# Kernel optimization log

Measured on AMD Instinct MI355X. Metric: run time of the kernel, lower is better.

The kernel has to match this reference:

```python
import jax, jax.numpy as jnp
import numpy as np

TAU = 2.0   # LIF membrane time constant
VTH = 1.0   # spike threshold
EPS = 1e-5
T = 2       # spiking timesteps
H = 8       # attention heads
L = 4       # transformer depth
SCALE = 0.125
GW = 0.8    # graph branch weight


def _spike(v):
    # heaviside forward, sigmoid surrogate backward (spikingjelly-style)
    sg = jax.nn.sigmoid(4.0 * (v - VTH))
    return sg + jax.lax.stop_gradient((v >= VTH).astype(v.dtype) - sg)


def lif(x):
    # multi-step LIF over leading time axis, hard reset, detach_reset=True
    def step(v, xt):
        v = v + (xt - v) / TAU
        s = _spike(v)
        v = v * (1.0 - jax.lax.stop_gradient(s))
        return v, s
    _, s = jax.lax.scan(step, jnp.zeros_like(x[0]), x)
    return s


def bn(x, g, b):
    # batch-norm (training stats) over all dims but the channel dim
    ax = tuple(range(x.ndim - 1))
    m = x.mean(ax, keepdims=True)
    v = x.var(ax, keepdims=True)
    return (x - m) * jax.lax.rsqrt(v + EPS) * g + b


def ln(x, g, b):
    m = x.mean(-1, keepdims=True)
    v = x.var(-1, keepdims=True)
    return (x - m) * jax.lax.rsqrt(v + EPS) * g + b


def gcn_agg(x, row, col, n):
    # symmetric-normalized sparse aggregation: out[col] += x[row] / sqrt(d[row]d[col])
    deg = jax.ops.segment_sum(jnp.ones_like(col, dtype=x.dtype), col, num_segments=n)
    dinv = jnp.where(deg > 0, jax.lax.rsqrt(deg), 0.0)
    val = dinv[col] * dinv[row]
    return jax.ops.segment_sum(val[:, None] * x[row], col, num_segments=n)


def _forward(fl, edge_index):
    (x, fc0_w, fc0_b, ln_g, ln_b, wq, wk, wv, wo,
     bnq_g, bnq_b, bnk_g, bnk_b, bnv_g, bnv_b, bno_g, bno_b,
     w1, bn1_g, bn1_b, w2, bn2_g, bn2_b, head_w, head_b,
     gfc_w, gfc_b, gbn0_g, gbn0_b, gconv_w, gconv_b, gbn_g, gbn_b,
     fc_w, fc_b) = fl
    N = x.shape[0]
    row, col = edge_index[0], edge_index[1]
    # ---- spiking transformer branch: x -> [T,N,D] ----
    h = jnp.broadcast_to(x, (T,) + x.shape) @ fc0_w + fc0_b
    h = jax.nn.relu(ln(h, ln_g, ln_b))
    D = h.shape[-1]
    for l in range(L):
        s = lif(h)
        q = lif(bn(s @ wq[l], bnq_g[l], bnq_b[l])).reshape(T, N, H, D // H)
        k = lif(bn(s @ wk[l], bnk_g[l], bnk_b[l])).reshape(T, N, H, D // H)
        v = lif(bn(s @ wv[l], bnv_g[l], bnv_b[l])).reshape(T, N, H, D // H)
        # linear (token-sum) spiking self-attention: kv = K^T V per head/timestep
        kv = jnp.einsum('tnhd,tnhe->thde', k, v)
        o = (jnp.einsum('tnhd,thde->tnhe', q, kv) * SCALE).reshape(T, N, D)
        o = bn(lif(o) @ wo[l], bno_g[l], bno_b[l])
        h = h + o
        m = bn(lif(h) @ w1[l], bn1_g[l], bn1_b[l])
        m = bn(lif(m) @ w2[l], bn2_g[l], bn2_b[l])
        h = h + m
    x1 = (lif(h) @ head_w + head_b).mean(0)   # [N, C], mean over T (TET=False)
    # ---- sparse GNN diffusion branch ----
    g0 = jax.nn.relu(bn(x @ gfc_w + gfc_b, gbn0_g, gbn0_b))
    g = g0
    for i in range(2):
        g = gcn_agg(g, row, col, N) @ gconv_w[i] + gconv_b[i]
        g = jax.nn.relu(bn(g, gbn_g[i], gbn_b[i]))
        g = g + g0  # residual to first layer
    out = GW * g + (1.0 - GW) * x1
    return out @ fc_w + fc_b


def setup_inputs() -> dict:
    key = jax.random.key(0)
    ks = iter(jax.random.split(key, 64))
    N, F, D, C = 16384, 512, 512, 40
    DH = 2 * D
    r = lambda *s: jax.random.normal(next(ks), s, dtype=jnp.float32)
    inp = {
        'x': r(N, F),
        'fc0_w': r(F, D) * 0.02, 'fc0_b': jnp.zeros((D,), jnp.float32),
        'ln_g': jnp.ones((D,), jnp.float32), 'ln_b': jnp.zeros((D,), jnp.float32),
        'wq': r(L, D, D) * 0.02, 'wk': r(L, D, D) * 0.02,
        'wv': r(L, D, D) * 0.02, 'wo': r(L, D, D) * 0.02,
        'bnq_g': 1.0 + 0.1 * r(L, D), 'bnq_b': 0.02 * r(L, D),
        'bnk_g': 1.0 + 0.1 * r(L, D), 'bnk_b': 0.02 * r(L, D),
        'bnv_g': 1.0 + 0.1 * r(L, D), 'bnv_b': 0.02 * r(L, D),
        'bno_g': 1.0 + 0.1 * r(L, D), 'bno_b': 0.02 * r(L, D),
        'w1': r(L, D, DH) * 0.02, 'bn1_g': 1.0 + 0.1 * r(L, DH), 'bn1_b': 0.02 * r(L, DH),
        'w2': r(L, DH, D) * 0.02, 'bn2_g': 1.0 + 0.1 * r(L, D), 'bn2_b': 0.02 * r(L, D),
        'head_w': r(D, C) * 0.02, 'head_b': jnp.zeros((C,), jnp.float32),
        'gfc_w': r(F, C) * 0.02, 'gfc_b': jnp.zeros((C,), jnp.float32),
        'gbn0_g': jnp.ones((C,), jnp.float32), 'gbn0_b': jnp.zeros((C,), jnp.float32),
        'gconv_w': r(2, C, C) * 0.1, 'gconv_b': jnp.zeros((2, C), jnp.float32),
        'gbn_g': 1.0 + 0.1 * r(2, C), 'gbn_b': 0.02 * r(2, C),
        'fc_w': r(C, C) * 0.1, 'fc_b': jnp.zeros((C,), jnp.float32),
        'edge_index': jax.random.randint(next(ks), (2, 262144), 0, N, dtype=jnp.int32),
    }
    return inp


def reference(x, fc0_w, fc0_b, ln_g, ln_b, wq, wk, wv, wo, bnq_g, bnq_b, bnk_g, bnk_b, bnv_g, bnv_b, bno_g, bno_b, w1, bn1_g, bn1_b, w2, bn2_g, bn2_b, head_w, head_b, gfc_w, gfc_b, gbn0_g, gbn0_b, gconv_w, gconv_b, gbn_g, gbn_b, fc_w, fc_b, edge_index):
    fl = (x, fc0_w, fc0_b, ln_g, ln_b, wq, wk, wv, wo, bnq_g, bnq_b, bnk_g, bnk_b, bnv_g, bnv_b, bno_g, bno_b, w1, bn1_g, bn1_b, w2, bn2_g, bn2_b, head_w, head_b, gfc_w, gfc_b, gbn0_g, gbn0_b, gconv_w, gconv_b, gbn_g, gbn_b, fc_w, fc_b)
    return _forward(fl, edge_index)
```

## Files before the change

### kernel.cpp

```cpp
#include <hip/hip_runtime.h>
#include <cstddef>
#include <cstdint>

constexpr int N_NODES = 16384;
constexpr int D_MODEL = 512;
constexpr int C_OUT   = 40;
constexpr int CW      = 256;
constexpr int ND      = N_NODES * D_MODEL;
constexpr int M2      = 2 * N_NODES;

typedef int i32x4 __attribute__((ext_vector_type(4)));

#define S0 0.001953125
#define S1 1.52587890625e-05
#define S2 1.1920928955078125e-07
#define S3 9.31322574615478515625e-10
#define S4 7.2759576141834259033203125e-12

#define WD_Q 0
#define WD_K 1310720
#define WD_V 2621440
#define WD_O 3932160
#define WD_1 5242880
#define WD_2 7864320
#define WD_TOTAL 10485760

__global__ __launch_bounds__(256)
void w_digits_layer(const float* __restrict__ wq, const float* __restrict__ wk,
                    const float* __restrict__ wv, const float* __restrict__ wo,
                    const float* __restrict__ w1, const float* __restrict__ w2,
                    uint8_t* __restrict__ Wd) {
    int idx = blockIdx.x * 256 + threadIdx.x;
    const float* W;
    uint8_t* outb;
    int N, rem;
    if (idx < 65536) {
        int mm = idx >> 14;
        rem = idx & 16383;
        const float* ptrs[4] = {wq, wk, wv, wo};
        W = ptrs[mm]; outb = Wd + (size_t)mm * 1310720; N = 512;
    } else if (idx < 98304) {
        rem = idx - 65536; W = w1; outb = Wd + WD_1; N = 1024;
    } else {
        rem = idx - 98304; W = w2; outb = Wd + WD_2; N = 512;
    }
    int kg = rem / N, n = rem - kg * N;
    const float* Wp = W + (size_t)kg * 16 * N + n;
    uint8_t* out = outb + (size_t)(kg * N + n) * 80;
    const double scl[5] = {512.0, 65536.0, 8388608.0, 1073741824.0, 137438953472.0};
    const double inv[5] = {S0, S1, S2, S3, S4};
    union { uint8_t b[5][16]; i32x4 v[5]; } db;
#pragma unroll
    for (int kk = 0; kk < 16; ++kk) {
        double r = (double)Wp[(size_t)kk * N];
#pragma unroll
        for (int j = 0; j < 5; ++j) {
            int d = (int)rint(r * scl[j]);
            d = d > 127 ? 127 : (d < -127 ? -127 : d);
            r -= (double)d * inv[j];
            db.b[j][kk] = (uint8_t)(int8_t)d;
        }
    }
#pragma unroll
    for (int j = 0; j < 5; ++j)
        *reinterpret_cast<i32x4*>(out + j * 16) = db.v[j];
}

__global__ __launch_bounds__(256)
void gemm_i8_bits(const uint64_t* __restrict__ bits, int kWords,
                  const uint8_t* __restrict__ Wd, int Nmat, int colOff,
                  float* __restrict__ C, int ldc, int K,
                  double* __restrict__ sum, double* __restrict__ sumsq) {
    __shared__ __attribute__((aligned(16))) uint8_t Bs[20480];
    const int lane = threadIdx.x & 63;
    const int wv   = threadIdx.x >> 6;
    const int m    = lane & 15;
    const int q    = lane >> 4;
    const int rowT = blockIdx.y * 128 + wv * 32;
    const int colB = blockIdx.x * 64;

    i32x4 acc[2][4][5];
#pragma unroll
    for (int rt = 0; rt < 2; ++rt)
#pragma unroll
        for (int t = 0; t < 4; ++t)
#pragma unroll
            for (int j = 0; j < 5; ++j) acc[rt][t][j] = (i32x4){0, 0, 0, 0};

    const uint64_t* brow0 = bits + (size_t)(rowT + m) * kWords;
    const uint64_t* brow1 = brow0 + (size_t)16 * kWords;
    const size_t cb = (size_t)(colOff + colB);

    for (int kb = 0; kb < K; kb += 64) {
        i32x4 tmp[5];
        const size_t kt0 = (size_t)(kb >> 4);
#pragma unroll
        for (int c5 = 0; c5 < 5; ++c5) {
            int c  = threadIdx.x + c5 * 256;
            int kt = c / 320;
            int of = c - kt * 320;
            tmp[c5] = *reinterpret_cast<const i32x4*>(
                Wd + ((kt0 + (size_t)kt) * Nmat + cb) * 80 + (size_t)of * 16);
        }
        uint64_t wb0 = brow0[kb >> 6];
        uint64_t wb1 = brow1[kb >> 6];
        uint32_t hw0 = (uint32_t)(wb0 >> (q * 16)) & 0xFFFFu;
        uint32_t hw1 = (uint32_t)(wb1 >> (q * 16)) & 0xFFFFu;
        i32x4 af0, af1;
#pragma unroll
        for (int i = 0; i < 4; ++i) {
            af0[i] = (int)((((hw0 >> (4 * i)) & 0xFu) * 0x00204081u) & 0x01010101u);
            af1[i] = (int)((((hw1 >> (4 * i)) & 0xFu) * 0x00204081u) & 0x01010101u);
        }
        __syncthreads();
#pragma unroll
        for (int c5 = 0; c5 < 5; ++c5) {
            int c  = threadIdx.x + c5 * 256;
            int kt = c / 320;
            int of = c - kt * 320;
            *reinterpret_cast<i32x4*>(Bs + kt * 5120 + of * 16) = tmp[c5];
        }
        __syncthreads();
#pragma unroll
        for (int t = 0; t < 4; ++t) {
            const uint8_t* bt = Bs + q * 5120 + (t * 16 + m) * 80;
            i32x4 bf[5];
#pragma unroll
            for (int j = 0; j < 5; ++j)
                bf[j] = *reinterpret_cast<const i32x4*>(bt + j * 16);
#pragma unroll
            for (int j = 0; j < 5; ++j) {
                acc[0][t][j] = __builtin_amdgcn_mfma_i32_16x16x64_i8(af0, bf[j], acc[0][t][j], 0, 0, 0);
                acc[1][t][j] = __builtin_amdgcn_mfma_i32_16x16x64_i8(af1, bf[j], acc[1][t][j], 0, 0, 0);
            }
        }
    }

    double sarr[4], qarr[4];
#pragma unroll
    for (int t = 0; t < 4; ++t) { sarr[t] = 0.0; qarr[t] = 0.0; }
#pragma unroll
    for (int rt = 0; rt < 2; ++rt) {
        const int orow = rowT + rt * 16 + q * 4;
#pragma unroll
        for (int t = 0; t < 4; ++t) {
            float* Cc = C + (size_t)orow * ldc + colB + t * 16 + m;
#pragma unroll
            for (int i = 0; i < 4; ++i) {
                double p = (double)acc[rt][t][0][i] * S0 + (double)acc[rt][t][1][i] * S1
                         + (double)acc[rt][t][2][i] * S2 + (double)acc[rt][t][3][i] * S3
                         + (double)acc[rt][t][4][i] * S4;
                Cc[(size_t)i * ldc] = (float)p;
                sarr[t] += p; qarr[t] += p * p;
            }
        }
    }
    __shared__ double ls[4][64], lq[4][64];
#pragma unroll
    for (int t = 0; t < 4; ++t) {
        double s = sarr[t], qq = qarr[t];
        s  += __shfl_xor(s, 16);  s  += __shfl_xor(s, 32);
        qq += __shfl_xor(qq, 16); qq += __shfl_xor(qq, 32);
        if (lane < 16) { ls[wv][t * 16 + lane] = s; lq[wv][t * 16 + lane] = qq; }
    }
    __syncthreads();
    if (threadIdx.x < 64) {
        int t = threadIdx.x;
        double s  = ls[0][t] + ls[1][t] + ls[2][t] + ls[3][t];
        double qq = lq[0][t] + lq[1][t] + lq[2][t] + lq[3][t];
        atomicAdd(&sum[colB + t], s);
        atomicAdd(&sumsq[colB + t], qq);
    }
}

__global__ __launch_bounds__(256)
void head_gather(const uint64_t* __restrict__ bits, const float* __restrict__ W,
                 const float* __restrict__ bias, float* __restrict__ Y) {
    const int lane = threadIdx.x & 63;
    const int wid  = threadIdx.x >> 6;
    const int r = blockIdx.x * 4 + wid;
    if (lane >= C_OUT) return;
    double acc = (double)bias[lane];
    const uint64_t* bw = bits + (size_t)r * 8;
    for (int j = 0; j < 8; ++j) {
        uint64_t w = bw[j];
        const float* Wk = W + (size_t)j * 64 * C_OUT + lane;
        while (w) {
            int k = __builtin_ctzll(w);
            w &= w - 1;
            acc += (double)Wk[(size_t)k * C_OUT];
        }
    }
    Y[(size_t)r * C_OUT + lane] = (float)acc;
}

__global__ __launch_bounds__(256)
void gemm_f32d(const float* __restrict__ A, int lda,
               const float* __restrict__ B, int ldb,
               const float* __restrict__ bias,
               double* __restrict__ C, int ldc, int M, int Nc, int K) {
    __shared__ float As[16][64];
    __shared__ float Bs[16][64];
    const int tid = threadIdx.x;
    const int tx  = tid & 15, ty = tid >> 4;
    const int row0 = blockIdx.y * 64 + ty * 4;
    const int col0 = blockIdx.x * 64 + tx * 4;
    const int ar = tid >> 2, ak = (tid & 3) * 4;
    const int bk = tid >> 4, bn = (tid & 15) * 4;
    const int gm = blockIdx.y * 64 + ar;
    double acc[4][4];
#pragma unroll
    for (int i = 0; i < 4; i++)
#pragma unroll
        for (int j = 0; j < 4; j++) acc[i][j] = 0.0;
    for (int k0 = 0; k0 < K; k0 += 16) {
        float4 av = *reinterpret_cast<const float4*>(&A[(size_t)gm * lda + k0 + ak]);
        const float* avp = reinterpret_cast<const float*>(&av);
#pragma unroll
        for (int j = 0; j < 4; j++)
            As[ak + j][ar ^ ((ak + j) & 12)] = avp[j];
        float4 bv = *reinterpret_cast<const float4*>(
            &B[(size_t)(k0 + bk) * ldb + blockIdx.x * 64 + bn]);
        *reinterpret_cast<float4*>(&Bs[bk][bn ^ ((bk & 3) << 2)]) = bv;
        __syncthreads();
#pragma unroll
        for (int kk = 0; kk < 16; kk++) {
            float4 a4 = *reinterpret_cast<const float4*>(&As[kk][(ty * 4) ^ (kk & 12)]);
            float4 b4 = *reinterpret_cast<const float4*>(&Bs[kk][(tx * 4) ^ ((kk & 3) << 2)]);
            const float* ap = reinterpret_cast<const float*>(&a4);
            const float* bp = reinterpret_cast<const float*>(&b4);
#pragma unroll
            for (int i = 0; i < 4; i++)
#pragma unroll
                for (int j = 0; j < 4; j++)
                    acc[i][j] = fma((double)ap[i], (double)bp[j], acc[i][j]);
        }
        __syncthreads();
    }
#pragma unroll
    for (int i = 0; i < 4; i++) {
        int r = row0 + i;
        if (r >= M) continue;
#pragma unroll
        for (int j = 0; j < 4; j++) {
            int c = col0 + j;
            if (c < Nc) {
                double v = acc[i][j];
                if (bias) v += (double)bias[c];
                C[(size_t)r * ldc + c] = v;
            }
        }
    }
}

__global__ __launch_bounds__(256)
void gemm_f32(const float* __restrict__ A, int lda,
              const float* __restrict__ B, int ldb,
              const float* __restrict__ bias,
              float* __restrict__ C, int ldc, int M, int Nc, int K) {
    __shared__ float As[16][64];
    __shared__ float Bs[16][64];
    const int tid = threadIdx.x;
    const int tx  = tid & 15, ty = tid >> 4;
    const int row0 = blockIdx.y * 64 + ty * 4;
    const int col0 = blockIdx.x * 64 + tx * 4;
    const int ar = tid >> 2, ak = (tid & 3) * 4;
    const int bk = tid >> 4, bn = (tid & 15) * 4;
    const int gm = blockIdx.y * 64 + ar;
    double acc[4][4];
#pragma unroll
    for (int i = 0; i < 4; i++)
#pragma unroll
        for (int j = 0; j < 4; j++) acc[i][j] = 0.0;
    for (int k0 = 0; k0 < K; k0 += 16) {
#pragma unroll
        for (int j = 0; j < 4; j++) {
            int kk = k0 + ak + j;
            As[ak + j][ar] = (gm < M && kk < K) ? A[(size_t)gm * lda + kk] : 0.f;
        }
#pragma unroll
        for (int j = 0; j < 4; j++) {
            int gn = blockIdx.x * 64 + bn + j;
            int kk = k0 + bk;
            Bs[bk][bn + j] = (gn < Nc && kk < K) ? B[(size_t)kk * ldb + gn] : 0.f;
        }
        __syncthreads();
#pragma unroll
        for (int kk = 0; kk < 16; kk++) {
            float a4[4], b4[4];
#pragma unroll
            for (int i = 0; i < 4; i++) a4[i] = As[kk][ty * 4 + i];
#pragma unroll
            for (int j = 0; j < 4; j++) b4[j] = Bs[kk][tx * 4 + j];
#pragma unroll
            for (int i = 0; i < 4; i++)
#pragma unroll
                for (int j = 0; j < 4; j++) acc[i][j] = fma((double)a4[i], (double)b4[j], acc[i][j]);
        }
        __syncthreads();
    }
#pragma unroll
    for (int i = 0; i < 4; i++) {
        int r = row0 + i;
        if (r >= M) continue;
#pragma unroll
        for (int j = 0; j < 4; j++) {
            int c = col0 + j;
            if (c < Nc) {
                double v = acc[i][j];
                if (bias) v += (double)bias[c];
                C[(size_t)r * ldc + c] = (float)v;
            }
        }
    }
}

__global__ __launch_bounds__(256)
void col_stats_f(const float* __restrict__ X, int M, int Ch, int rowsPerBlock,
                 double* __restrict__ sum, double* __restrict__ sumsq) {
    const int cl = threadIdx.x & 63;
    const int c  = blockIdx.x * 64 + cl;
    const int rg = threadIdx.x >> 6;
    const int r0 = blockIdx.y * rowsPerBlock;
    const int r1 = min(r0 + rowsPerBlock, M);
    double s = 0.0, q = 0.0;
    if (c < Ch) {
        for (int r = r0 + rg; r < r1; r += 4) {
            double v = (double)X[(size_t)r * Ch + c];
            s += v; q += v * v;
        }
    }
    __shared__ double ls[4][64], lq[4][64];
    ls[rg][cl] = s; lq[rg][cl] = q;
    __syncthreads();
    if (rg == 0 && c < Ch) {
        s = ls[0][cl] + ls[1][cl] + ls[2][cl] + ls[3][cl];
        q = lq[0][cl] + lq[1][cl] + lq[2][cl] + lq[3][cl];
        atomicAdd(&sum[c], s);
        atomicAdd(&sumsq[c], q);
    }
}

__device__ __forceinline__ void lif2(double x0, double x1, bool& s0, bool& s1) {
    double v = x0 * 0.5;
    s0 = (v >= 1.0);
    v = s0 ? 0.0 : v;
    v = v + (x1 - v) * 0.5;
    s1 = (v >= 1.0);
}

__device__ __forceinline__ void bn_params(const double* sum, const double* sumsq,
                                          const float* g, const float* b, double invM,
                                          int c, double& sc, double& sh) {
    double m   = sum[c] * invM;
    double var = sumsq[c] * invM - m * m;
    sc = (double)g[c] / sqrt(var + 1e-5);
    sh = (double)b[c] - m * sc;
}

__global__ __launch_bounds__(256)
void bn_lif_bits2(const float* __restrict__ X,
                  const double* __restrict__ sum, const double* __restrict__ sumsq,
                  const float* __restrict__ g, const float* __restrict__ b, double invM,
                  uint64_t* __restrict__ S, int osWords, int chOffWords) {
    int i = blockIdx.x * 256 + threadIdx.x;
    int n = i >> 8, c = i & 255;
    double sc, sh;
    bn_params(sum, sumsq, g, b, invM, c, sc, sh);
    bool s0, s1;
    lif2((double)X[i] * sc + sh, (double)X[(size_t)i + (size_t)N_NODES * 256] * sc + sh, s0, s1);
    uint64_t b0 = __ballot(s0), b1 = __ballot(s1);
    if ((threadIdx.x & 63) == 0) {
        int widx = n * osWords + chOffWords + (c >> 6);
        S[widx] = b0;
        S[widx + N_NODES * osWords] = b1;
    }
}

__global__ __launch_bounds__(256)
void bn_add_lif2(const float* __restrict__ X,
                 const double* __restrict__ sum, const double* __restrict__ sumsq,
                 const float* __restrict__ g, const float* __restrict__ b, double invM,
                 double* __restrict__ H, int chOff, uint64_t* __restrict__ S) {
    int i = blockIdx.x * 256 + threadIdx.x;
    int n = i >> 8, c = i & 255;
    double sc, sh;
    bn_params(sum, sumsq, g, b, invM, c, sc, sh);
    size_t hi = (size_t)n * 512 + chOff + c;
    double h0 = H[hi] + ((double)X[i] * sc + sh);
    double h1 = H[hi + ND] + ((double)X[(size_t)i + (size_t)N_NODES * 256] * sc + sh);
    H[hi] = h0;
    H[hi + ND] = h1;
    bool s0, s1;
    lif2(h0, h1, s0, s1);
    uint64_t b0 = __ballot(s0), b1 = __ballot(s1);
    if ((threadIdx.x & 63) == 0) {
        int widx = n * 8 + (chOff >> 6) + (c >> 6);
        S[widx] = b0;
        S[widx + N_NODES * 8] = b1;
    }
}

__global__ __launch_bounds__(256)
void ln_relu_lif(const double* __restrict__ X, const float* __restrict__ g,
                 const float* __restrict__ b, double* __restrict__ H,
                 uint64_t* __restrict__ S) {
    int n = blockIdx.x;
    const double* x = X + (size_t)n * 512;
    int c0 = threadIdx.x, c1 = threadIdx.x + 256;
    double v0 = x[c0], v1 = x[c1];
    __shared__ double ls[256], lq[256];
    ls[threadIdx.x] = v0 + v1;
    lq[threadIdx.x] = v0 * v0 + v1 * v1;
    __syncthreads();
    for (int off = 128; off > 0; off >>= 1) {
        if (threadIdx.x < off) {
            ls[threadIdx.x] += ls[threadIdx.x + off];
            lq[threadIdx.x] += lq[threadIdx.x + off];
        }
        __syncthreads();
    }
    double m    = ls[0] * (1.0 / 512);
    double var  = lq[0] * (1.0 / 512) - m * m;
    double rstd = 1.0 / sqrt(var + 1e-5);
    double o0 = (v0 - m) * rstd * (double)g[c0] + (double)b[c0];
    double o1 = (v1 - m) * rstd * (double)g[c1] + (double)b[c1];
    o0 = o0 > 0.0 ? o0 : 0.0;
    o1 = o1 > 0.0 ? o1 : 0.0;
    double* h0 = H + (size_t)n * 512;
    h0[c0] = o0; h0[c1] = o1;
    h0[ND + c0] = o0; h0[ND + c1] = o1;
    bool a0, a1, d0, d1;
    lif2(o0, o0, a0, a1);
    lif2(o1, o1, d0, d1);
    uint64_t ba0 = __ballot(a0), ba1 = __ballot(a1);
    uint64_t bd0 = __ballot(d0), bd1 = __ballot(d1);
    if ((threadIdx.x & 63) == 0) {
        int w = threadIdx.x >> 6;
        S[n * 8 + w] = ba0;
        S[n * 8 + w + N_NODES * 8] = ba1;
        S[n * 8 + 4 + w] = bd0;
        S[n * 8 + 4 + w + N_NODES * 8] = bd1;
    }
}

__global__ __launch_bounds__(256)
void kv_bits(const uint64_t* __restrict__ Kb, const uint64_t* __restrict__ Vb,
             float* __restrict__ KV, int nPerBlock) {
    const int th = blockIdx.x;
    const int t = th >> 3, h = th & 7;
    const int nbase = blockIdx.y * nPerBlock;
    const int e = threadIdx.x & 63, dg = threadIdx.x >> 6;
    float acc[16];
#pragma unroll
    for (int i = 0; i < 16; i++) acc[i] = 0.f;
    __shared__ float ks[16][64], vs[16][64];
    const size_t wbase = (size_t)t * N_NODES * 8 + h;
    for (int n0 = 0; n0 < nPerBlock; n0 += 16) {
        for (int idx = threadIdx.x; idx < 16 * 128; idx += 256) {
            int r = idx >> 7, c = idx & 127;
            size_t wi = wbase + (size_t)(nbase + n0 + r) * 8;
            if (c < 64) ks[r][c] = (float)((Kb[wi] >> c) & 1ull);
            else        vs[r][c - 64] = (float)((Vb[wi] >> (c - 64)) & 1ull);
        }
        __syncthreads();
#pragma unroll
        for (int r = 0; r < 16; ++r) {
            float ve = vs[r][e];
#pragma unroll
            for (int i = 0; i < 16; ++i) acc[i] += ks[r][dg * 16 + i] * ve;
        }
        __syncthreads();
    }
    float* kvp = KV + (size_t)th * 4096;
    for (int i = 0; i < 16; ++i)
        atomicAdd(&kvp[(dg * 16 + i) * 64 + e], acc[i]);
}

__global__ __launch_bounds__(256)
void o_lif_bits(const uint64_t* __restrict__ Qb, const float* __restrict__ KV,
                uint64_t* __restrict__ S) {
    const int h  = blockIdx.y;
    const int nb = blockIdx.x;
    __shared__ float kvs[64][64];
    __shared__ float qs[64][65];
    const int e = threadIdx.x & 63, rg = threadIdx.x >> 6;
    float acc0[16], acc1[16];
#pragma unroll
    for (int i = 0; i < 16; ++i) { acc0[i] = 0.f; acc1[i] = 0.f; }
#pragma unroll
    for (int t = 0; t < 2; ++t) {
        const float* kvp = KV + (size_t)(t * 8 + h) * 4096;
        for (int idx = threadIdx.x; idx < 4096; idx += 256)
            kvs[idx >> 6][idx & 63] = kvp[idx];
        const size_t wbase = ((size_t)t * N_NODES + (size_t)nb * 64) * 8 + h;
        for (int idx = threadIdx.x; idx < 4096; idx += 256) {
            int r = idx >> 6, c = idx & 63;
            qs[r][c] = (float)((Qb[wbase + (size_t)r * 8] >> c) & 1ull);
        }
        __syncthreads();
        float* acc = t == 0 ? acc0 : acc1;
        for (int d = 0; d < 64; ++d) {
            float kv = kvs[d][e];
#pragma unroll
            for (int i = 0; i < 16; ++i) acc[i] += qs[rg * 16 + i][d] * kv;
        }
        __syncthreads();
    }
#pragma unroll
    for (int i = 0; i < 16; ++i) {
        float o0 = acc0[i] * 0.125f;
        float o1 = acc1[i] * 0.125f;
        bool s0, s1;
        lif2((double)o0, (double)o1, s0, s1);
        uint64_t b0 = __ballot(s0), b1 = __ballot(s1);
        if (e == 0) {
            size_t row = (size_t)nb * 64 + rg * 16 + i;
            S[row * 8 + h] = b0;
            S[row * 8 + h + (size_t)N_NODES * 8] = b1;
        }
    }
}

__global__ __launch_bounds__(256)
void deg_kernel(const int* __restrict__ col, float* __restrict__ deg, int E) {
    int e = blockIdx.x * 256 + threadIdx.x;
    if (e < E) atomicAdd(&deg[col[e]], 1.0f);
}

__global__ __launch_bounds__(256)
void dinv_kernel(float* __restrict__ deg, int n) {
    int i = blockIdx.x * 256 + threadIdx.x;
    if (i < n) {
        double d = (double)deg[i];
        deg[i] = d > 0.0 ? (float)(1.0 / sqrt(d)) : 0.f;
    }
}

__global__ __launch_bounds__(256)
void agg_kernel(const float* __restrict__ G, const int* __restrict__ row,
                const int* __restrict__ col, const float* __restrict__ dinv,
                float* __restrict__ out, int E) {
    int idx = blockIdx.x * 256 + threadIdx.x;
    int e = idx / C_OUT, c = idx - e * C_OUT;
    if (e >= E) return;
    int r = row[e], cl = col[e];
    float val = dinv[cl] * dinv[r];
    atomicAdd(&out[(size_t)cl * C_OUT + c], val * G[(size_t)r * C_OUT + c]);
}

__global__ __launch_bounds__(256)
void bn_relu_add_f2(const float* __restrict__ X,
                    const double* __restrict__ sum, const double* __restrict__ sumsq,
                    const float* __restrict__ g, const float* __restrict__ b, double invM,
                    const float* __restrict__ add, float* __restrict__ out, int NC, int Ch) {
    int i = blockIdx.x * 256 + threadIdx.x;
    if (i >= NC) return;
    int c = i % Ch;
    double sc, sh;
    bn_params(sum, sumsq, g, b, invM, c, sc, sh);
    double v = (double)X[i] * sc + sh;
    v = v > 0.0 ? v : 0.0;
    if (add) v += (double)add[i];
    out[i] = (float)v;
}

__global__ __launch_bounds__(256)
void mix_kernel(const float* __restrict__ G, const float* __restrict__ Y,
                float* __restrict__ P, int NC) {
    int i = blockIdx.x * 256 + threadIdx.x;
    if (i >= NC) return;
    double y = 0.5 * ((double)Y[i] + (double)Y[(size_t)i + NC]);
    P[i] = (float)(0.8 * (double)G[i] + 0.2 * y);
}

__global__ __launch_bounds__(256)
void final_fc_kernel(const float* __restrict__ A, const float* __restrict__ W,
                     const float* __restrict__ bias, float* __restrict__ out) {
    __shared__ float Ws[40][40];
    for (int idx = threadIdx.x; idx < 1600; idx += 256)
        Ws[idx / 40][idx % 40] = W[idx];
    __syncthreads();
    int i = blockIdx.x * 256 + threadIdx.x;
    if (i >= N_NODES * C_OUT) return;
    int n = i / 40, c = i - n * 40;
    const float* a = A + (size_t)n * 40;
    double acc = (double)bias[c];
#pragma unroll 8
    for (int k = 0; k < 40; ++k) acc += (double)a[k] * (double)Ws[k][c];
    out[i] = (float)acc;
}

static inline dim3 grid1(long n) { return dim3((unsigned)((n + 255) / 256)); }

extern "C" void kernel_launch(void* const* d_in, const int* in_sizes, int n_in,
                              void* d_out, int out_size, void* d_ws, size_t ws_size,
                              hipStream_t stream) {
    const float* x      = (const float*)d_in[0];
    const float* fc0_w  = (const float*)d_in[1];
    const float* fc0_b  = (const float*)d_in[2];
    const float* ln_g   = (const float*)d_in[3];
    const float* ln_b   = (const float*)d_in[4];
    const float* wq     = (const float*)d_in[5];
    const float* wk     = (const float*)d_in[6];
    const float* wv     = (const float*)d_in[7];
    const float* wo     = (const float*)d_in[8];
    const float* bnq_g  = (const float*)d_in[9];
    const float* bnq_b  = (const float*)d_in[10];
    const float* bnk_g  = (const float*)d_in[11];
    const float* bnk_b  = (const float*)d_in[12];
    const float* bnv_g  = (const float*)d_in[13];
    const float* bnv_b  = (const float*)d_in[14];
    const float* bno_g  = (const float*)d_in[15];
    const float* bno_b  = (const float*)d_in[16];
    const float* w1     = (const float*)d_in[17];
    const float* bn1_g  = (const float*)d_in[18];
    const float* bn1_b  = (const float*)d_in[19];
    const float* w2     = (const float*)d_in[20];
    const float* bn2_g  = (const float*)d_in[21];
    const float* bn2_b  = (const float*)d_in[22];
    const float* head_w = (const float*)d_in[23];
    const float* head_b = (const float*)d_in[24];
    const float* gfc_w  = (const float*)d_in[25];
    const float* gfc_b  = (const float*)d_in[26];
    const float* gbn0_g = (const float*)d_in[27];
    const float* gbn0_b = (const float*)d_in[28];
    const float* gconv_w= (const float*)d_in[29];
    const float* gconv_b= (const float*)d_in[30];
    const float* gbn_g  = (const float*)d_in[31];
    const float* gbn_b  = (const float*)d_in[32];
    const float* fc_w   = (const float*)d_in[33];
    const float* fc_b   = (const float*)d_in[34];
    const int*   edge   = (const int*)d_in[35];

    const int E = in_sizes[35] / 2;
    const int* erow = edge;
    const int* ecol = edge + E;
    const int NC = N_NODES * C_OUT;

    uint8_t* wsbase = (uint8_t*)d_ws;
    size_t off = 0;
    auto alloc = [&](size_t bytes, size_t align) -> void* {
        off = (off + align - 1) & ~(align - 1);
        void* p = wsbase + off;
        off += bytes;
        return p;
    };
    double*   statBuf = (double*)alloc((size_t)64 * 512 * sizeof(double), 256);
    double*   h_buf  = (double*)alloc((size_t)2 * ND * sizeof(double), 256);
    double*   Pd     = (double*)alloc((size_t)M2 * CW * sizeof(double), 256);
    float*    Pf     = (float*)Pd;
    uint8_t*  Wdig   = (uint8_t*)alloc((size_t)WD_TOTAL, 256);
    uint64_t* s_bits = (uint64_t*)alloc((size_t)2 * N_NODES * 8 * 8, 256);
    uint64_t* q_bits = (uint64_t*)alloc((size_t)2 * N_NODES * 8 * 8, 256);
    uint64_t* k_bits = (uint64_t*)alloc((size_t)2 * N_NODES * 8 * 8, 256);
    uint64_t* v_bits = (uint64_t*)alloc((size_t)2 * N_NODES * 8 * 8, 256);
    uint64_t* m_bits = (uint64_t*)alloc((size_t)2 * N_NODES * 16 * 8, 256);
    float*    ybuf   = (float*)m_bits;
    (void)alloc((size_t)2 * NC * sizeof(float) > (size_t)2 * N_NODES * 16 * 8
                ? (size_t)2 * NC * sizeof(float) - (size_t)2 * N_NODES * 16 * 8 : 0, 256);
    float*    g0     = (float*)alloc((size_t)NC * sizeof(float), 256);
    float*    gg     = (float*)alloc((size_t)NC * sizeof(float), 256);
    float*    ag     = (float*)alloc((size_t)NC * sizeof(float), 256);
    float*    kvb    = (float*)alloc((size_t)65536 * sizeof(float), 256);
    float*    deg    = (float*)alloc((size_t)N_NODES * sizeof(float), 256);
    if (off > ws_size) return;

    const dim3 blk(256);
    const dim3 gCHK((unsigned)(N_NODES));
    const dim3 gGEMM(CW / 64, M2 / 128);
    const double invM2 = 1.0 / (double)M2;
    const double invMN = 1.0 / (double)N_NODES;

    hipMemsetAsync(statBuf, 0, (size_t)64 * 512 * sizeof(double), stream);

    int gate = 0;
    auto nextStat = [&]() { return statBuf + (size_t)(gate++) * 512; };

    hipLaunchKernelGGL(gemm_f32d, dim3(8, N_NODES / 64), blk, 0, stream,
                       x, 512, fc0_w, 512, fc0_b, Pd, 512, N_NODES, 512, 512);
    hipLaunchKernelGGL(ln_relu_lif, dim3(N_NODES), blk, 0, stream, Pd, ln_g, ln_b, h_buf, s_bits);

    for (int l = 0; l < 4; ++l) {
        hipLaunchKernelGGL(w_digits_layer, dim3(512), blk, 0, stream,
                           wq + (size_t)l * 262144, wk + (size_t)l * 262144,
                           wv + (size_t)l * 262144, wo + (size_t)l * 262144,
                           w1 + (size_t)l * 524288, w2 + (size_t)l * 524288, Wdig);

        uint64_t* qkvb[3] = {q_bits, k_bits, v_bits};
        const size_t wdoff[3] = {WD_Q, WD_K, WD_V};
        const float* gmat[3] = {bnq_g + l * 512, bnk_g + l * 512, bnv_g + l * 512};
        const float* bmat[3] = {bnq_b + l * 512, bnk_b + l * 512, bnv_b + l * 512};
        for (int j = 0; j < 3; ++j) {
            for (int c0 = 0; c0 < 512; c0 += CW) {
                double* st = nextStat();
                hipLaunchKernelGGL(gemm_i8_bits, gGEMM, blk, 0, stream,
                                   s_bits, 8, Wdig + wdoff[j], 512, c0, Pf, CW, 512, st, st + 256);
                hipLaunchKernelGGL(bn_lif_bits2, gCHK, blk, 0, stream,
                                   Pf, st, st + 256, gmat[j] + c0, bmat[j] + c0, invM2,
                                   qkvb[j], 8, c0 / 64);
            }
        }

        hipMemsetAsync(kvb, 0, 65536 * sizeof(float), stream);
        hipLaunchKernelGGL(kv_bits, dim3(16, 16), blk, 0, stream, k_bits, v_bits, kvb, 1024);
        hipLaunchKernelGGL(o_lif_bits, dim3(N_NODES / 64, 8), blk, 0, stream, q_bits, kvb, q_bits);

        for (int c0 = 0; c0 < 512; c0 += CW) {
            double* st = nextStat();
            hipLaunchKernelGGL(gemm_i8_bits, gGEMM, blk, 0, stream,
                               q_bits, 8, Wdig + WD_O, 512, c0, Pf, CW, 512, st, st + 256);
            hipLaunchKernelGGL(bn_add_lif2, gCHK, blk, 0, stream,
                               Pf, st, st + 256, bno_g + l * 512 + c0, bno_b + l * 512 + c0,
                               invM2, h_buf, c0, s_bits);
        }

        for (int c0 = 0; c0 < 1024; c0 += CW) {
            double* st = nextStat();
            hipLaunchKernelGGL(gemm_i8_bits, gGEMM, blk, 0, stream,
                               s_bits, 8, Wdig + WD_1, 1024, c0, Pf, CW, 512, st, st + 256);
            hipLaunchKernelGGL(bn_lif_bits2, gCHK, blk, 0, stream,
                               Pf, st, st + 256, bn1_g + l * 1024 + c0, bn1_b + l * 1024 + c0,
                               invM2, m_bits, 16, c0 / 64);
        }
        for (int c0 = 0; c0 < 512; c0 += CW) {
            double* st = nextStat();
            hipLaunchKernelGGL(gemm_i8_bits, gGEMM, blk, 0, stream,
                               m_bits, 16, Wdig + WD_2, 512, c0, Pf, CW, 1024, st, st + 256);
            hipLaunchKernelGGL(bn_add_lif2, gCHK, blk, 0, stream,
                               Pf, st, st + 256, bn2_g + l * 512 + c0, bn2_b + l * 512 + c0,
                               invM2, h_buf, c0, s_bits);
        }
    }

    hipLaunchKernelGGL(head_gather, dim3(M2 / 4), blk, 0, stream, s_bits, head_w, head_b, ybuf);

    hipLaunchKernelGGL(gemm_f32, dim3(1, N_NODES / 64), blk, 0, stream,
                       x, 512, gfc_w, 40, gfc_b, ag, 40, N_NODES, 40, 512);
    {
        double* st = nextStat();
        dim3 gs(1, (N_NODES + 511) / 512);
        hipLaunchKernelGGL(col_stats_f, gs, blk, 0, stream, ag, N_NODES, 40, 512, st, st + 256);
        hipLaunchKernelGGL(bn_relu_add_f2, grid1(NC), blk, 0, stream,
                           ag, st, st + 256, gbn0_g, gbn0_b, invMN,
                           (const float*)nullptr, g0, NC, 40);
    }

    hipMemsetAsync(deg, 0, N_NODES * sizeof(float), stream);
    hipLaunchKernelGGL(deg_kernel, grid1(E), blk, 0, stream, ecol, deg, E);
    hipLaunchKernelGGL(dinv_kernel, grid1(N_NODES), blk, 0, stream, deg, N_NODES);

    const float* gsrc = g0;
    for (int i = 0; i < 2; ++i) {
        hipMemsetAsync(ag, 0, (size_t)NC * sizeof(float), stream);
        hipLaunchKernelGGL(agg_kernel, grid1((long)E * C_OUT), blk, 0, stream,
                           gsrc, erow, ecol, deg, ag, E);
        hipLaunchKernelGGL(gemm_f32, dim3(1, N_NODES / 64), blk, 0, stream,
                           ag, 40, gconv_w + (size_t)i * 40 * 40, 40, gconv_b + i * 40,
                           gg, 40, N_NODES, 40, 40);
        double* st = nextStat();
        dim3 gs(1, (N_NODES + 511) / 512);
        hipLaunchKernelGGL(col_stats_f, gs, blk, 0, stream, gg, N_NODES, 40, 512, st, st + 256);
        hipLaunchKernelGGL(bn_relu_add_f2, grid1(NC), blk, 0, stream,
                           gg, st, st + 256, gbn_g + i * 40, gbn_b + i * 40, invMN, g0, gg, NC, 40);
        gsrc = gg;
    }

    hipLaunchKernelGGL(mix_kernel, grid1(NC), blk, 0, stream, gg, ybuf, ag, NC);
    hipLaunchKernelGGL(final_fc_kernel, grid1((long)N_NODES * C_OUT), blk, 0, stream,
                       ag, fc_w, fc_b, (float*)d_out);
}
```

Baseline: 6.283 ms.

## Process full 512-column chunks and store residual stream as fp32

Replaces the 256-column chunking of the spiking GEMM plus BN/LIF passes with full 512-column launches, halving the number of GEMM and BN kernel launches and re-reads of the bit-packed spike inputs. The residual buffer h and the fc0 output change from double to float, halving their memory traffic, while arithmetic stays in double. The cost is a larger Pf scratch buffer and possible threshold-crossing differences from rounding h to fp32 between layers.

Measured after the change: 5.815 ms. 1.08x faster.

```diff
diff --git a/kernel.cpp b/kernel.cpp
--- a/kernel.cpp
+++ b/kernel.cpp
@@ -5,7 +5,6 @@
 constexpr int N_NODES = 16384;
 constexpr int D_MODEL = 512;
 constexpr int C_OUT   = 40;
-constexpr int CW      = 256;
 constexpr int ND      = N_NODES * D_MODEL;
 constexpr int M2      = 2 * N_NODES;
 
@@ -198,7 +197,7 @@
 void gemm_f32d(const float* __restrict__ A, int lda,
                const float* __restrict__ B, int ldb,
                const float* __restrict__ bias,
-               double* __restrict__ C, int ldc, int M, int Nc, int K) {
+               float* __restrict__ C, int ldc, int M, int Nc, int K) {
     __shared__ float As[16][64];
     __shared__ float Bs[16][64];
     const int tid = threadIdx.x;
@@ -247,7 +246,7 @@
             if (c < Nc) {
                 double v = acc[i][j];
                 if (bias) v += (double)bias[c];
-                C[(size_t)r * ldc + c] = v;
+                C[(size_t)r * ldc + c] = (float)v;
             }
         }
     }
@@ -364,11 +363,11 @@
                   const float* __restrict__ g, const float* __restrict__ b, double invM,
                   uint64_t* __restrict__ S, int osWords, int chOffWords) {
     int i = blockIdx.x * 256 + threadIdx.x;
-    int n = i >> 8, c = i & 255;
+    int n = i >> 9, c = i & 511;
     double sc, sh;
     bn_params(sum, sumsq, g, b, invM, c, sc, sh);
     bool s0, s1;
-    lif2((double)X[i] * sc + sh, (double)X[(size_t)i + (size_t)N_NODES * 256] * sc + sh, s0, s1);
+    lif2((double)X[i] * sc + sh, (double)X[(size_t)i + (size_t)ND] * sc + sh, s0, s1);
     uint64_t b0 = __ballot(s0), b1 = __ballot(s1);
     if ((threadIdx.x & 63) == 0) {
         int widx = n * osWords + chOffWords + (c >> 6);
@@ -381,34 +380,33 @@
 void bn_add_lif2(const float* __restrict__ X,
                  const double* __restrict__ sum, const double* __restrict__ sumsq,
                  const float* __restrict__ g, const float* __restrict__ b, double invM,
-                 double* __restrict__ H, int chOff, uint64_t* __restrict__ S) {
+                 float* __restrict__ H, uint64_t* __restrict__ S) {
     int i = blockIdx.x * 256 + threadIdx.x;
-    int n = i >> 8, c = i & 255;
+    int n = i >> 9, c = i & 511;
     double sc, sh;
     bn_params(sum, sumsq, g, b, invM, c, sc, sh);
-    size_t hi = (size_t)n * 512 + chOff + c;
-    double h0 = H[hi] + ((double)X[i] * sc + sh);
-    double h1 = H[hi + ND] + ((double)X[(size_t)i + (size_t)N_NODES * 256] * sc + sh);
-    H[hi] = h0;
-    H[hi + ND] = h1;
+    double h0 = (double)H[i] + ((double)X[i] * sc + sh);
+    double h1 = (double)H[(size_t)i + ND] + ((double)X[(size_t)i + ND] * sc + sh);
+    H[i] = (float)h0;
+    H[(size_t)i + ND] = (float)h1;
     bool s0, s1;
     lif2(h0, h1, s0, s1);
     uint64_t b0 = __ballot(s0), b1 = __ballot(s1);
     if ((threadIdx.x & 63) == 0) {
-        int widx = n * 8 + (chOff >> 6) + (c >> 6);
+        int widx = n * 8 + (c >> 6);
         S[widx] = b0;
         S[widx + N_NODES * 8] = b1;
     }
 }
 
 __global__ __launch_bounds__(256)
-void ln_relu_lif(const double* __restrict__ X, const float* __restrict__ g,
-                 const float* __restrict__ b, double* __restrict__ H,
+void ln_relu_lif(const float* __restrict__ X, const float* __restrict__ g,
+                 const float* __restrict__ b, float* __restrict__ H,
                  uint64_t* __restrict__ S) {
     int n = blockIdx.x;
-    const double* x = X + (size_t)n * 512;
+    const float* x = X + (size_t)n * 512;
     int c0 = threadIdx.x, c1 = threadIdx.x + 256;
-    double v0 = x[c0], v1 = x[c1];
+    double v0 = (double)x[c0], v1 = (double)x[c1];
     __shared__ double ls[256], lq[256];
     ls[threadIdx.x] = v0 + v1;
     lq[threadIdx.x] = v0 * v0 + v1 * v1;
@@ -427,9 +425,9 @@
     double o1 = (v1 - m) * rstd * (double)g[c1] + (double)b[c1];
     o0 = o0 > 0.0 ? o0 : 0.0;
     o1 = o1 > 0.0 ? o1 : 0.0;
-    double* h0 = H + (size_t)n * 512;
-    h0[c0] = o0; h0[c1] = o1;
-    h0[ND + c0] = o0; h0[ND + c1] = o1;
+    float* h0 = H + (size_t)n * 512;
+    h0[c0] = (float)o0; h0[c1] = (float)o1;
+    h0[ND + c0] = (float)o0; h0[ND + c1] = (float)o1;
     bool a0, a1, d0, d1;
     lif2(o0, o0, a0, a1);
     lif2(o1, o1, d0, d1);
@@ -646,10 +644,9 @@
         off += bytes;
         return p;
     };
-    double*   statBuf = (double*)alloc((size_t)64 * 512 * sizeof(double), 256);
-    double*   h_buf  = (double*)alloc((size_t)2 * ND * sizeof(double), 256);
-    double*   Pd     = (double*)alloc((size_t)M2 * CW * sizeof(double), 256);
-    float*    Pf     = (float*)Pd;
+    double*   statBuf = (double*)alloc((size_t)64 * 1024 * sizeof(double), 256);
+    float*    h_buf  = (float*)alloc((size_t)2 * ND * sizeof(float), 256);
+    float*    Pf     = (float*)alloc((size_t)M2 * 512 * sizeof(float), 256);
     uint8_t*  Wdig   = (uint8_t*)alloc((size_t)WD_TOTAL, 256);
     uint64_t* s_bits = (uint64_t*)alloc((size_t)2 * N_NODES * 8 * 8, 256);
     uint64_t* q_bits = (uint64_t*)alloc((size_t)2 * N_NODES * 8 * 8, 256);
@@ -667,19 +664,19 @@
     if (off > ws_size) return;
 
     const dim3 blk(256);
-    const dim3 gCHK((unsigned)(N_NODES));
-    const dim3 gGEMM(CW / 64, M2 / 128);
+    const dim3 gBN((unsigned)(2 * N_NODES));
+    const dim3 gGEMM(8, M2 / 128);
     const double invM2 = 1.0 / (double)M2;
     const double invMN = 1.0 / (double)N_NODES;
 
-    hipMemsetAsync(statBuf, 0, (size_t)64 * 512 * sizeof(double), stream);
+    hipMemsetAsync(statBuf, 0, (size_t)64 * 1024 * sizeof(double), stream);
 
     int gate = 0;
-    auto nextStat = [&]() { return statBuf + (size_t)(gate++) * 512; };
+    auto nextStat = [&]() { return statBuf + (size_t)(gate++) * 1024; };
 
     hipLaunchKernelGGL(gemm_f32d, dim3(8, N_NODES / 64), blk, 0, stream,
-                       x, 512, fc0_w, 512, fc0_b, Pd, 512, N_NODES, 512, 512);
-    hipLaunchKernelGGL(ln_relu_lif, dim3(N_NODES), blk, 0, stream, Pd, ln_g, ln_b, h_buf, s_bits);
+                       x, 512, fc0_w, 512, fc0_b, Pf, 512, N_NODES, 512, 512);
+    hipLaunchKernelGGL(ln_relu_lif, dim3(N_NODES), blk, 0, stream, Pf, ln_g, ln_b, h_buf, s_bits);
 
     for (int l = 0; l < 4; ++l) {
         hipLaunchKernelGGL(w_digits_layer, dim3(512), blk, 0, stream,
@@ -692,44 +689,41 @@
         const float* gmat[3] = {bnq_g + l * 512, bnk_g + l * 512, bnv_g + l * 512};
         const float* bmat[3] = {bnq_b + l * 512, bnk_b + l * 512, bnv_b + l * 512};
         for (int j = 0; j < 3; ++j) {
-            for (int c0 = 0; c0 < 512; c0 += CW) {
-                double* st = nextStat();
-                hipLaunchKernelGGL(gemm_i8_bits, gGEMM, blk, 0, stream,
-                                   s_bits, 8, Wdig + wdoff[j], 512, c0, Pf, CW, 512, st, st + 256);
-                hipLaunchKernelGGL(bn_lif_bits2, gCHK, blk, 0, stream,
-                                   Pf, st, st + 256, gmat[j] + c0, bmat[j] + c0, invM2,
-                                   qkvb[j], 8, c0 / 64);
-            }
+            double* st = nextStat();
+            hipLaunchKernelGGL(gemm_i8_bits, gGEMM, blk, 0, stream,
+                               s_bits, 8, Wdig + wdoff[j], 512, 0, Pf, 512, 512, st, st + 512);
+            hipLaunchKernelGGL(bn_lif_bits2, gBN, blk, 0, stream,
+                               Pf, st, st + 512, gmat[j], bmat[j], invM2, qkvb[j], 8, 0);
         }
 
         hipMemsetAsync(kvb, 0, 65536 * sizeof(float), stream);
         hipLaunchKernelGGL(kv_bits, dim3(16, 16), blk, 0, stream, k_bits, v_bits, kvb, 1024);
         hipLaunchKernelGGL(o_lif_bits, dim3(N_NODES / 64, 8), blk, 0, stream, q_bits, kvb, q_bits);
 
-        for (int c0 = 0; c0 < 512; c0 += CW) {
+        {
             double* st = nextStat();
             hipLaunchKernelGGL(gemm_i8_bits, gGEMM, blk, 0, stream,
-                               q_bits, 8, Wdig + WD_O, 512, c0, Pf, CW, 512, st, st + 256);
-            hipLaunchKernelGGL(bn_add_lif2, gCHK, blk, 0, stream,
-                               Pf, st, st + 256, bno_g + l * 512 + c0, bno_b + l * 512 + c0,
-                               invM2, h_buf, c0, s_bits);
-        }
-
-        for (int c0 = 0; c0 < 1024; c0 += CW) {
+                               q_bits, 8, Wdig + WD_O, 512, 0, Pf, 512, 512, st, st + 512);
+            hipLaunchKernelGGL(bn_add_lif2, gBN, blk, 0, stream,
+                               Pf, st, st + 512, bno_g + l * 512, bno_b + l * 512,
+                               invM2, h_buf, s_bits);
+        }
+
+        for (int c0 = 0; c0 < 1024; c0 += 512) {
             double* st = nextStat();
             hipLaunchKernelGGL(gemm_i8_bits, gGEMM, blk, 0, stream,
-                               s_bits, 8, Wdig + WD_1, 1024, c0, Pf, CW, 512, st, st + 256);
-            hipLaunchKernelGGL(bn_lif_bits2, gCHK, blk, 0, stream,
-                               Pf, st, st + 256, bn1_g + l * 1024 + c0, bn1_b + l * 1024 + c0,
+                               s_bits, 8, Wdig + WD_1, 1024, c0, Pf, 512, 512, st, st + 512);
+            hipLaunchKernelGGL(bn_lif_bits2, gBN, blk, 0, stream,
+                               Pf, st, st + 512, bn1_g + l * 1024 + c0, bn1_b + l * 1024 + c0,
                                invM2, m_bits, 16, c0 / 64);
         }
-        for (int c0 = 0; c0 < 512; c0 += CW) {
+        {
             double* st = nextStat();
             hipLaunchKernelGGL(gemm_i8_bits, gGEMM, blk, 0, stream,
-                               m_bits, 16, Wdig + WD_2, 512, c0, Pf, CW, 1024, st, st + 256);
-            hipLaunchKernelGGL(bn_add_lif2, gCHK, blk, 0, stream,
-                               Pf, st, st + 256, bn2_g + l * 512 + c0, bn2_b + l * 512 + c0,
-                               invM2, h_buf, c0, s_bits);
+                               m_bits, 16, Wdig + WD_2, 512, 0, Pf, 512, 1024, st, st + 512);
+            hipLaunchKernelGGL(bn_add_lif2, gBN, blk, 0, stream,
+                               Pf, st, st + 512, bn2_g + l * 512, bn2_b + l * 512,
+                               invM2, h_buf, s_bits);
         }
     }
 
@@ -740,9 +734,9 @@
     {
         double* st = nextStat();
         dim3 gs(1, (N_NODES + 511) / 512);
-        hipLaunchKernelGGL(col_stats_f, gs, blk, 0, stream, ag, N_NODES, 40, 512, st, st + 256);
+        hipLaunchKernelGGL(col_stats_f, gs, blk, 0, stream, ag, N_NODES, 40, 512, st, st + 512);
         hipLaunchKernelGGL(bn_relu_add_f2, grid1(NC), blk, 0, stream,
-                           ag, st, st + 256, gbn0_g, gbn0_b, invMN,
+                           ag, st, st + 512, gbn0_g, gbn0_b, invMN,
                            (const float*)nullptr, g0, NC, 40);
     }
 
@@ -760,9 +754,9 @@
                            gg, 40, N_NODES, 40, 40);
         double* st = nextStat();
         dim3 gs(1, (N_NODES + 511) / 512);
-        hipLaunchKernelGGL(col_stats_f, gs, blk, 0, stream, gg, N_NODES, 40, 512, st, st + 256);
+        hipLaunchKernelGGL(col_stats_f, gs, blk, 0, stream, gg, N_NODES, 40, 512, st, st + 512);
         hipLaunchKernelGGL(bn_relu_add_f2, grid1(NC), blk, 0, stream,
-                           gg, st, st + 256, gbn_g + i * 40, gbn_b + i * 40, invMN, g0, gg, NC, 40);
+                           gg, st, st + 512, gbn_g + i * 40, gbn_b + i * 40, invMN, g0, gg, NC, 40);
         gsrc = gg;
     }
 
```
